# Kernel optimization log

Hardware: AMD Instinct MI355X
Metric: run time of the kernel (lower is better)

Reference implementation:

```python
import jax, jax.numpy as jnp
from jax import lax
import numpy as np

S, B, HP, WP, CIN, CO, DS, DI, K = 6, 1, 37, 37, 1536, 256, 16, 512, 4
N = HP * WP          # 1369 patches (37x37 grid)
OH, OW = 148, 148
HID = max(S * CO // 4, S)  # 384, attention hidden


def setup_inputs() -> dict:
    key = jax.random.key(0)
    ks = iter(jax.random.split(key, 64))
    def nrm(shape, scale):
        return jax.random.normal(next(ks), shape, jnp.float32) * scale
    inp = {}
    inp["features"] = nrm((S, B, 1, N, CIN), 1.0)
    # AdaptiveFusionModule (global branch)
    inp["proj_w"] = nrm((S, CO, CIN), CIN ** -0.5)          # per-source 1x1 conv
    inp["attn_w1"] = nrm((S * CO, HID), (S * CO) ** -0.5)
    inp["attn_b1"] = jnp.zeros((HID,), jnp.float32)
    inp["attn_w2"] = nrm((HID, S), HID ** -0.5)
    inp["attn_b2"] = jnp.zeros((S,), jnp.float32)
    inp["src_scale"] = jnp.ones((S,), jnp.float32)
    # two SelectiveSSM parameter sets (fwd / bwd scan)
    def ssm_params(tag):
        d = {}
        d[tag + "_in_w"] = nrm((CO, 2 * DI), CO ** -0.5)
        d[tag + "_conv_w"] = nrm((K, DI), K ** -0.5)         # depthwise causal conv
        d[tag + "_conv_b"] = jnp.zeros((DI,), jnp.float32)
        d[tag + "_xp_w"] = nrm((DI, 2 * DS + DI + 1), 0.02)  # B, C, delta, dt_bias
        # trained A_log; scaled so the log-domain cumsum stays in fp32 range over L=1369
        d[tag + "_Alog"] = jnp.log(jnp.arange(1, DS + 1, dtype=jnp.float32) / 1000.0) * jnp.ones((DI, 1), jnp.float32)
        d[tag + "_D"] = jnp.ones((DI,), jnp.float32)
        d[tag + "_out_w"] = nrm((DI, CO), DI ** -0.5)
        d[tag + "_ln_g"] = jnp.ones((CO,), jnp.float32)
        d[tag + "_ln_b"] = jnp.zeros((CO,), jnp.float32)
        return d
    inp.update(ssm_params("f"))
    inp.update(ssm_params("b"))
    inp["merge_w"] = nrm((2 * CO, CO), (2 * CO) ** -0.5)     # MSSR merge 1x1 conv
    inp["co1_w"] = nrm((3, 3, CO, CO), (9 * CO) ** -0.5)     # conv_out1, HWIO
    inp["co1_b"] = jnp.zeros((CO,), jnp.float32)
    inp["hp"], inp["wp"], inp["out_h"], inp["out_w"] = HP, WP, OH, OW
    return inp


def _causal_dwconv(z, w, b):
    # z: [B,L,D], w: [K,D] -> torch Conv1d(groups=D, padding=K-1)[..., :L]
    Kk, L = w.shape[0], z.shape[1]
    zp = jnp.pad(z, ((0, 0), (Kk - 1, 0), (0, 0)))
    return sum(zp[:, k:k + L, :] * w[k] for k in range(Kk)) + b


def _ssm(x, in_w, conv_w, conv_b, xp_w, Alog, D, out_w, ln_g, ln_b):
    # x: [B,L,d_model] -> [B,L,d_model]
    z, gate = jnp.split(x @ in_w, 2, axis=-1)               # [B,L,DI] each
    z = jax.nn.silu(_causal_dwconv(z, conv_w, conv_b))
    xp = z @ xp_w                                           # [B,L,2*DS+DI+1]
    ds = Alog.shape[1]
    Bp, Cp = xp[..., :ds], xp[..., ds:2 * ds]
    delta = jax.nn.softplus(xp[..., 2 * ds:-1] + xp[..., -1:])  # [B,L,DI]
    dA = jnp.exp(delta[..., None] * (-jnp.exp(Alog)))       # [B,L,DI,DS]
    dBu = delta[..., None] * Bp[:, :, None, :] * z[..., None]
    # log-domain cumsum scan: h[t] = sum_s exp(cs[t]-cs[s]) * dBu[s]
    cs = jnp.cumsum(jnp.log(jnp.clip(dA, 1e-38)), axis=1)
    h = jnp.exp(cs) * jnp.cumsum(jnp.exp(-cs) * dBu, axis=1)
    y = (h * Cp[:, :, None, :]).sum(-1) + D * z             # [B,L,DI]
    y = (y * jax.nn.silu(gate)) @ out_w                     # [B,L,d_model]
    r = y + x                                               # residual + LayerNorm
    mu = r.mean(-1, keepdims=True)
    v = ((r - mu) ** 2).mean(-1, keepdims=True)
    return ln_g * (r - mu) * lax.rsqrt(v + 1e-5) + ln_b


def _forward(features, proj_w, attn_w1, attn_b1, attn_w2, attn_b2, src_scale,
             f_in_w, f_conv_w, f_conv_b, f_xp_w, f_Alog, f_D, f_out_w, f_ln_g, f_ln_b,
             b_in_w, b_conv_w, b_conv_b, b_xp_w, b_Alog, b_D, b_out_w, b_ln_g, b_ln_b,
             merge_w, co1_w, co1_b, hp, wp, out_h, out_w):
    feats = features[:, :, 0]                               # [S,B,N,Cin]
    pf = jnp.einsum('sbnc,soc->sbno', feats, proj_w)        # [S,B,N,Co] per-source 1x1 proj
    Bsz = pf.shape[1]
    concat = pf.mean(2).transpose(1, 0, 2).reshape(Bsz, -1)  # [B,S*Co] pooled concat
    w = jax.nn.softmax(jax.nn.relu(concat @ attn_w1 + attn_b1) @ attn_w2 + attn_b2, axis=-1)
    w = jax.nn.softmax(w * src_scale, axis=-1)              # double softmax as in torch
    fused = jnp.einsum('bs,sbnc->bnc', w, pf)               # [B,N,Co]
    # MSSR bidirectional scan over row-major flattened patches
    fwd = _ssm(fused, f_in_w, f_conv_w, f_conv_b, f_xp_w, f_Alog, f_D, f_out_w, f_ln_g, f_ln_b)
    bwd = _ssm(fused[:, ::-1], b_in_w, b_conv_w, b_conv_b, b_xp_w, b_Alog, b_D, b_out_w, b_ln_g, b_ln_b)[:, ::-1]
    out = jnp.concatenate([fwd, bwd], axis=-1) @ merge_w    # [B,N,Co]
    sp = out.reshape(Bsz, hp, wp, -1)                       # NHWC
    up = jax.image.resize(sp, (Bsz, out_h, out_w, sp.shape[-1]), method='bilinear')
    y = lax.conv_general_dilated(up, co1_w, (1, 1), 'SAME',
                                 dimension_numbers=('NHWC', 'HWIO', 'NHWC')) + co1_b
    return y.transpose(0, 3, 1, 2)                          # [B,Co,out_h,out_w]


def reference(features, proj_w, attn_w1, attn_b1, attn_w2, attn_b2, src_scale,
              f_in_w, f_conv_w, f_conv_b, f_xp_w, f_Alog, f_D, f_out_w, f_ln_g, f_ln_b,
              b_in_w, b_conv_w, b_conv_b, b_xp_w, b_Alog, b_D, b_out_w, b_ln_g, b_ln_b,
              merge_w, co1_w, co1_b, hp, wp, out_h, out_w):
    return _forward(features, proj_w, attn_w1, attn_b1, attn_w2, attn_b2, src_scale,
                    f_in_w, f_conv_w, f_conv_b, f_xp_w, f_Alog, f_D, f_out_w, f_ln_g, f_ln_b,
                    b_in_w, b_conv_w, b_conv_b, b_xp_w, b_Alog, b_D, b_out_w, b_ln_g, b_ln_b,
                    merge_w, co1_w, co1_b, hp, wp, out_h, out_w)
```

## Files before the change

kernel.cpp:

```cpp
#include <hip/hip_runtime.h>
#include <math.h>


namespace {
constexpr int kS   = 6;
constexpr int kHP  = 37;
constexpr int kWP  = 37;
constexpr int kN   = 1369;
constexpr int kCIN = 1536;
constexpr int kCO  = 256;
constexpr int kDS  = 16;
constexpr int kDI  = 512;
constexpr int kHID = 384;
constexpr int kOH  = 148;
constexpr int kOW  = 148;
constexpr int kNP  = kOH * kOW;
constexpr int kXPW = 545;
constexpr long kXPS = 746112;
constexpr int kNC  = 48;
constexpr int kCH  = 29;

constexpr long OFF_PF      = 0;
constexpr long OFF_Z2B     = 0;
constexpr long OFF_YGB     = 0;
constexpr long OFF_UPB     = 0;
constexpr long OFF_SCANP   = 700928;
constexpr long OFF_SCANH   = 1487360;
constexpr long OFF_COLPART = 2102784;
constexpr long OFF_WFIN    = 2119680;
constexpr long OFF_ATTNP   = 2119696;
constexpr long OFF_PROJWB  = 2200000;
constexpr long OFF_INWT    = 2200000;
constexpr long OFF_FUSEDB  = 2462144;
constexpr long OFF_ZG      = 2820624;
constexpr long OFF_Z       = 5760000;
constexpr long OFF_WCONVB  = 6000000;
constexpr long OFF_FEATB   = 7161856;
constexpr long OFF_XP      = 7161856;
constexpr long OFF_DELTA   = 8654080;
constexpr long OFF_OUTWT   = 10055936;
constexpr long OFF_GT      = 11457792;
constexpr long OFF_XPWT    = 11457792;
constexpr long OFF_FUSED2  = 12158720;
constexpr long OFF_CAT     = 12859648;
constexpr long OFF_MERGEWT = 13210112;
constexpr long OFF_MERGED  = 13560576;
}

typedef __attribute__((ext_vector_type(8))) short bf16x8;
typedef __attribute__((ext_vector_type(4))) float f32x4;

__device__ __forceinline__ short f2bf(float x) {
    unsigned u = __builtin_bit_cast(unsigned, x);
    unsigned r = u + 0x7fffu + ((u >> 16) & 1u);
    return (short)(r >> 16);
}

__device__ __forceinline__ bf16x8 cvt8(float4 x, float4 y) {
    union { short s[8]; bf16x8 v; } u;
    u.s[0] = f2bf(x.x); u.s[1] = f2bf(x.y); u.s[2] = f2bf(x.z); u.s[3] = f2bf(x.w);
    u.s[4] = f2bf(y.x); u.s[5] = f2bf(y.y); u.s[6] = f2bf(y.z); u.s[7] = f2bf(y.w);
    return u.v;
}

__global__ __launch_bounds__(256)
void cast8_kernel(const float* __restrict__ in, short* __restrict__ out, long n8)
{
    long i = (long)blockIdx.x * 256 + threadIdx.x;
    if (i >= n8) return;
    const float4* p = (const float4*)(in + i * 8);
    *(bf16x8*)(out + i * 8) = cvt8(p[0], p[1]);
}

__global__ __launch_bounds__(256)
void transpose_cast_kernel(const float* __restrict__ w0, const float* __restrict__ w1,
                           short* __restrict__ wt, int K, int N)
{
    __shared__ float tile[32][33];
    int dir = blockIdx.z;
    const float* w = dir ? w1 : w0;
    short* o = wt + (long)dir * K * N;
    int k0 = blockIdx.x * 32, n0 = blockIdx.y * 32;
    int tx = threadIdx.x & 31, ty = threadIdx.x >> 5;
    #pragma unroll
    for (int r = 0; r < 32; r += 8) {
        int k = k0 + ty + r, n = n0 + tx;
        tile[ty + r][tx] = (k < K && n < N) ? w[(long)k * N + n] : 0.f;
    }
    __syncthreads();
    #pragma unroll
    for (int r = 0; r < 32; r += 8) {
        int n = n0 + ty + r, k = k0 + tx;
        if (n < N && k < K) o[(long)n * K + k] = f2bf(tile[tx][ty + r]);
    }
}

__global__ __launch_bounds__(256)
void mfma_nt(const short* __restrict__ A, long sA,
             const short* __restrict__ B, long sB,
             float* __restrict__ C, long sC,
             int M, int N, int K)
{
    __shared__ short smem[2][8192];
    const int bz = blockIdx.z;
    const short* Ab = A + (long)bz * sA;
    const short* Bb = B + (long)bz * sB;
    float* Cb = C + (long)bz * sC;
    const int t = threadIdx.x, w = t >> 6, l = t & 63;
    const int lr = l & 15, sg = l >> 4;
    const int m0 = blockIdx.x * 64, n0 = blockIdx.y * 64;

    const int srow = t >> 3, qa = t & 7;
    long gA[2]; int woffA[2];
    #pragma unroll
    for (int j = 0; j < 2; ++j) {
        int ar = srow + j * 32;
        int am = m0 + ar; if (am >= M) am = M - 1;
        gA[j] = (long)am * K + qa * 8;
        woffA[j] = ar * 128 + ((qa ^ (ar & 7)) << 4);
    }
    long gB[2]; int woffB[2];
    #pragma unroll
    for (int j = 0; j < 2; ++j) {
        int br = srow + j * 32;
        int bn = n0 + br; if (bn >= N) bn = N - 1;
        gB[j] = (long)bn * K + qa * 8;
        woffB[j] = 8192 + br * 128 + ((qa ^ (br & 7)) << 4);
    }

    int aoff[2][2], boff[2][2];
    #pragma unroll
    for (int mi = 0; mi < 2; ++mi) {
        int r = (w >> 1) * 32 + mi * 16 + lr;
        #pragma unroll
        for (int kk = 0; kk < 2; ++kk)
            aoff[mi][kk] = r * 128 + (((kk * 4 + sg) ^ (r & 7)) << 4);
    }
    #pragma unroll
    for (int ni = 0; ni < 2; ++ni) {
        int r = (w & 1) * 32 + ni * 16 + lr;
        #pragma unroll
        for (int kk = 0; kk < 2; ++kk)
            boff[ni][kk] = 8192 + r * 128 + (((kk * 4 + sg) ^ (r & 7)) << 4);
    }

    f32x4 acc[2][2] = {};
    const int NT = K >> 6;
    {
        char* lb = (char*)&smem[0][0];
        #pragma unroll
        for (int j = 0; j < 2; ++j)
            *(bf16x8*)(lb + woffA[j]) = *(const bf16x8*)(Ab + gA[j]);
        #pragma unroll
        for (int j = 0; j < 2; ++j)
            *(bf16x8*)(lb + woffB[j]) = *(const bf16x8*)(Bb + gB[j]);
    }
    __syncthreads();
    for (int tt = 0; tt < NT; ++tt) {
        bf16x8 nsa[2], nsb[2];
        if (tt + 1 < NT) {
            long o = (long)(tt + 1) * 64;
            #pragma unroll
            for (int j = 0; j < 2; ++j) nsa[j] = *(const bf16x8*)(Ab + gA[j] + o);
            #pragma unroll
            for (int j = 0; j < 2; ++j) nsb[j] = *(const bf16x8*)(Bb + gB[j] + o);
        }
        char* lb = (char*)&smem[tt & 1][0];
        #pragma unroll
        for (int kk = 0; kk < 2; ++kk) {
            bf16x8 a[2], b[2];
            #pragma unroll
            for (int mi = 0; mi < 2; ++mi) a[mi] = *(const bf16x8*)(lb + aoff[mi][kk]);
            #pragma unroll
            for (int ni = 0; ni < 2; ++ni) b[ni] = *(const bf16x8*)(lb + boff[ni][kk]);
            #pragma unroll
            for (int mi = 0; mi < 2; ++mi)
                #pragma unroll
                for (int ni = 0; ni < 2; ++ni)
                    acc[mi][ni] = __builtin_amdgcn_mfma_f32_16x16x32_bf16(a[mi], b[ni], acc[mi][ni], 0, 0, 0);
        }
        if (tt + 1 < NT) {
            char* nb = (char*)&smem[(tt + 1) & 1][0];
            #pragma unroll
            for (int j = 0; j < 2; ++j) *(bf16x8*)(nb + woffA[j]) = nsa[j];
            #pragma unroll
            for (int j = 0; j < 2; ++j) *(bf16x8*)(nb + woffB[j]) = nsb[j];
        }
        __syncthreads();
    }
    const int q = l >> 4;
    const int wm0 = m0 + (w >> 1) * 32, wn0 = n0 + (w & 1) * 32;
    #pragma unroll
    for (int mi = 0; mi < 2; ++mi)
        #pragma unroll
        for (int ni = 0; ni < 2; ++ni)
            #pragma unroll
            for (int r = 0; r < 4; ++r) {
                int m = wm0 + mi * 16 + q * 4 + r;
                int n = wn0 + ni * 16 + lr;
                if (m < M && n < N)
                    Cb[(long)m * N + n] = acc[mi][ni][r];
            }
}

__global__ __launch_bounds__(256)
void proj_mfma_kernel(const short* __restrict__ Ab16, const short* __restrict__ Bb16,
                      float* __restrict__ pf)
{
    __shared__ short smem[2][8192];
    const int bid = blockIdx.x;
    const int slot = (bid & 7) * 66 + (bid >> 3);
    const int s = slot / 88, rem = slot - s * 88;
    const int m0 = (rem >> 2) * 64, n0 = (rem & 3) * 64;
    const short* A = Ab16 + (long)s * kN * kCIN;
    const short* B = Bb16 + (long)s * kCO * kCIN;
    float* C = pf + (long)s * kN * kCO;
    const int t = threadIdx.x, w = t >> 6, l = t & 63;
    const int lr = l & 15, sg = l >> 4;

    const int srow = t >> 3, qa = t & 7;
    long gA[2]; int woffA[2];
    #pragma unroll
    for (int j = 0; j < 2; ++j) {
        int ar = srow + j * 32;
        int am = m0 + ar; if (am >= kN) am = kN - 1;
        gA[j] = (long)am * kCIN + qa * 8;
        woffA[j] = ar * 128 + ((qa ^ (ar & 7)) << 4);
    }
    long gB[2]; int woffB[2];
    #pragma unroll
    for (int j = 0; j < 2; ++j) {
        int br = srow + j * 32;
        gB[j] = (long)(n0 + br) * kCIN + qa * 8;
        woffB[j] = 8192 + br * 128 + ((qa ^ (br & 7)) << 4);
    }

    int aoff[2][2], boff[2][2];
    #pragma unroll
    for (int mi = 0; mi < 2; ++mi) {
        int r = (w >> 1) * 32 + mi * 16 + lr;
        #pragma unroll
        for (int kk = 0; kk < 2; ++kk)
            aoff[mi][kk] = r * 128 + (((kk * 4 + sg) ^ (r & 7)) << 4);
    }
    #pragma unroll
    for (int ni = 0; ni < 2; ++ni) {
        int r = (w & 1) * 32 + ni * 16 + lr;
        #pragma unroll
        for (int kk = 0; kk < 2; ++kk)
            boff[ni][kk] = 8192 + r * 128 + (((kk * 4 + sg) ^ (r & 7)) << 4);
    }

    f32x4 acc[2][2] = {};
    const int NT = kCIN >> 6;
    {
        char* lb = (char*)&smem[0][0];
        #pragma unroll
        for (int j = 0; j < 2; ++j)
            *(bf16x8*)(lb + woffA[j]) = *(const bf16x8*)(A + gA[j]);
        #pragma unroll
        for (int j = 0; j < 2; ++j)
            *(bf16x8*)(lb + woffB[j]) = *(const bf16x8*)(B + gB[j]);
    }
    __syncthreads();
    for (int tt = 0; tt < NT; ++tt) {
        bf16x8 nsa[2], nsb[2];
        if (tt + 1 < NT) {
            long o = (long)(tt + 1) * 64;
            #pragma unroll
            for (int j = 0; j < 2; ++j) nsa[j] = *(const bf16x8*)(A + gA[j] + o);
            #pragma unroll
            for (int j = 0; j < 2; ++j) nsb[j] = *(const bf16x8*)(B + gB[j] + o);
        }
        char* lb = (char*)&smem[tt & 1][0];
        #pragma unroll
        for (int kk = 0; kk < 2; ++kk) {
            bf16x8 a[2], b[2];
            #pragma unroll
            for (int mi = 0; mi < 2; ++mi) a[mi] = *(const bf16x8*)(lb + aoff[mi][kk]);
            #pragma unroll
            for (int ni = 0; ni < 2; ++ni) b[ni] = *(const bf16x8*)(lb + boff[ni][kk]);
            #pragma unroll
            for (int mi = 0; mi < 2; ++mi)
                #pragma unroll
                for (int ni = 0; ni < 2; ++ni)
                    acc[mi][ni] = __builtin_amdgcn_mfma_f32_16x16x32_bf16(a[mi], b[ni], acc[mi][ni], 0, 0, 0);
        }
        if (tt + 1 < NT) {
            char* nb = (char*)&smem[(tt + 1) & 1][0];
            #pragma unroll
            for (int j = 0; j < 2; ++j) *(bf16x8*)(nb + woffA[j]) = nsa[j];
            #pragma unroll
            for (int j = 0; j < 2; ++j) *(bf16x8*)(nb + woffB[j]) = nsb[j];
        }
        __syncthreads();
    }
    const int q = l >> 4;
    const int wm0 = m0 + (w >> 1) * 32, wn0 = n0 + (w & 1) * 32;
    #pragma unroll
    for (int mi = 0; mi < 2; ++mi)
        #pragma unroll
        for (int ni = 0; ni < 2; ++ni)
            #pragma unroll
            for (int r = 0; r < 4; ++r) {
                int m = wm0 + mi * 16 + q * 4 + r;
                if (m < kN)
                    C[(long)m * kCO + wn0 + ni * 16 + lr] = acc[mi][ni][r];
            }
}

__global__ __launch_bounds__(256)
void conv_mfma_kernel(const short* __restrict__ up, const short* __restrict__ wt,
                      const float* __restrict__ bias, float* __restrict__ out)
{
    __shared__ short smem[2][12288];
    const int t = threadIdx.x, w = t >> 6, l = t & 63;
    const int lr = l & 15, sg = l >> 4;
    const int bid = blockIdx.x;
    const int xcd = bid & 7, slot = bid >> 3;
    const int wgid = (xcd < 6 ? xcd * 86 : 6 * 86 + (xcd - 6) * 85) + slot;
    const int pm0 = (wgid >> 1) * 64;
    const int bn0 = (wgid & 1) * 128;

    const int srow = t >> 3, qa = t & 7;
    long gA[2]; int woffA[2];
    #pragma unroll
    for (int j = 0; j < 2; ++j) {
        int ar = srow + j * 32;
        int p = pm0 + ar; if (p >= kNP) p = kNP - 1;
        int oy = p / kOW, ox = p - oy * kOW;
        gA[j] = ((long)oy * 150 + ox) * kCO + qa * 8;
        woffA[j] = ar * 128 + ((qa ^ (ar & 7)) << 4);
    }
    long gB[4]; int woffB[4];
    #pragma unroll
    for (int j = 0; j < 4; ++j) {
        int br = srow + j * 32;
        gB[j] = (long)(bn0 + br) * 2304 + qa * 8;
        woffB[j] = 8192 + br * 128 + ((qa ^ (br & 7)) << 4);
    }

    int aoff[2][2], boff[4][2];
    #pragma unroll
    for (int mi = 0; mi < 2; ++mi) {
        int r = (w >> 1) * 32 + mi * 16 + lr;
        #pragma unroll
        for (int kk = 0; kk < 2; ++kk)
            aoff[mi][kk] = r * 128 + (((kk * 4 + sg) ^ (r & 7)) << 4);
    }
    #pragma unroll
    for (int ni = 0; ni < 4; ++ni) {
        int r = (w & 1) * 64 + ni * 16 + lr;
        #pragma unroll
        for (int kk = 0; kk < 2; ++kk)
            boff[ni][kk] = 8192 + r * 128 + (((kk * 4 + sg) ^ (r & 7)) << 4);
    }

    f32x4 acc[2][4] = {};
    const int NT = 36;

#define CONV_BAR() { \
        asm volatile("s_waitcnt lgkmcnt(0)" ::: "memory"); \
        __builtin_amdgcn_sched_barrier(0); \
        __builtin_amdgcn_s_barrier(); }

#define CONV_TADDR(tn, ta, tb) { \
        int _tap = (tn) >> 2, _c0 = ((tn) & 3) << 6; \
        int _ky = _tap / 3, _kx = _tap - _ky * 3; \
        ta = ((long)_ky * 150 + _kx) * kCO + _c0; \
        tb = (long)(tn) * 64; }

#define CONV_LOAD(Pa_, Pb_, tn) { \
        long _ta, _tb; CONV_TADDR(tn, _ta, _tb); \
        _Pragma("unroll") \
        for (int j = 0; j < 2; ++j) Pa_[j] = *(const bf16x8*)(up + gA[j] + _ta); \
        _Pragma("unroll") \
        for (int j = 0; j < 4; ++j) Pb_[j] = *(const bf16x8*)(wt + gB[j] + _tb); }

#define CONV_WRITE(buf, Pa_, Pb_) { \
        char* _nb = (char*)&smem[buf][0]; \
        _Pragma("unroll") \
        for (int j = 0; j < 2; ++j) *(bf16x8*)(_nb + woffA[j]) = Pa_[j]; \
        _Pragma("unroll") \
        for (int j = 0; j < 4; ++j) *(bf16x8*)(_nb + woffB[j]) = Pb_[j]; }

#define CONV_COMPUTE(buf) { \
        char* _lb = (char*)&smem[buf][0]; \
        _Pragma("unroll") \
        for (int kk = 0; kk < 2; ++kk) { \
            bf16x8 _a[2], _b[4]; \
            _Pragma("unroll") \
            for (int mi = 0; mi < 2; ++mi) _a[mi] = *(const bf16x8*)(_lb + aoff[mi][kk]); \
            _Pragma("unroll") \
            for (int ni = 0; ni < 4; ++ni) _b[ni] = *(const bf16x8*)(_lb + boff[ni][kk]); \
            __builtin_amdgcn_s_setprio(1); \
            _Pragma("unroll") \
            for (int mi = 0; mi < 2; ++mi) \
                _Pragma("unroll") \
                for (int ni = 0; ni < 4; ++ni) \
                    acc[mi][ni] = __builtin_amdgcn_mfma_f32_16x16x32_bf16(_a[mi], _b[ni], acc[mi][ni], 0, 0, 0); \
            __builtin_amdgcn_s_setprio(0); \
        } }

    bf16x8 PaA[2], PaB[4];
    bf16x8 PbA[2], PbB[4];

    CONV_LOAD(PaA, PaB, 0);
    CONV_WRITE(0, PaA, PaB);
    CONV_LOAD(PbA, PbB, 1);
    CONV_BAR();

    for (int tt = 0; tt < NT; tt += 2) {
        if (tt + 2 < NT) CONV_LOAD(PaA, PaB, tt + 2);
        CONV_COMPUTE(0);
        CONV_WRITE(1, PbA, PbB);
        CONV_BAR();
        if (tt + 3 < NT) CONV_LOAD(PbA, PbB, tt + 3);
        CONV_COMPUTE(1);
        if (tt + 2 < NT) CONV_WRITE(0, PaA, PaB);
        CONV_BAR();
    }
#undef CONV_BAR
#undef CONV_TADDR
#undef CONV_LOAD
#undef CONV_WRITE
#undef CONV_COMPUTE

    const int q = l >> 4;
    const int m0 = pm0 + (w >> 1) * 32;
    const int n0 = bn0 + (w & 1) * 64;
    #pragma unroll
    for (int mi = 0; mi < 2; ++mi)
        #pragma unroll
        for (int ni = 0; ni < 4; ++ni) {
            const int co = n0 + ni * 16 + lr;
            const float bv = bias[co];
            #pragma unroll
            for (int r = 0; r < 4; ++r) {
                int p = m0 + mi * 16 + q * 4 + r;
                if (p < kNP)
                    out[(long)co * kNP + p] = acc[mi][ni][r] + bv;
            }
        }
}

__global__ __launch_bounds__(256)
void colmean_kernel(const float* __restrict__ pf, float* __restrict__ colpart)
{
    int s = blockIdx.x, ch = blockIdx.y, o = threadIdx.x;
    int n0 = ch * 128, n1 = n0 + 128 > kN ? kN : n0 + 128;
    float a = 0.f;
    for (int n = n0; n < n1; ++n) a += pf[((long)s * kN + n) * kCO + o];
    colpart[ch * kS * kCO + s * kCO + o] = a;
}

__global__ __launch_bounds__(384)
void attn_part1(const float* __restrict__ colpart, const float* __restrict__ w1,
                float* __restrict__ partial)
{
    __shared__ float cm[128];
    int b = blockIdx.x, t = threadIdx.x;
    int c0 = b * 128;
    if (t < 128) {
        float a = 0.f;
        #pragma unroll
        for (int ch = 0; ch < 11; ++ch) a += colpart[ch * kS * kCO + c0 + t];
        cm[t] = a * (1.f / kN);
    }
    __syncthreads();
    float acc = 0.f;
    #pragma unroll 4
    for (int c = 0; c < 128; ++c) acc += cm[c] * w1[(long)(c0 + c) * kHID + t];
    partial[b * kHID + t] = acc;
}

__global__ __launch_bounds__(384)
void attn_part2(const float* __restrict__ partial, const float* __restrict__ b1,
                const float* __restrict__ w2, const float* __restrict__ b2,
                const float* __restrict__ ss, float* __restrict__ wfin)
{
    __shared__ float h[kHID];
    __shared__ float logits[8];
    int t = threadIdx.x;
    float acc = b1[t];
    #pragma unroll
    for (int b = 0; b < 12; ++b) acc += partial[b * kHID + t];
    h[t] = fmaxf(acc, 0.f);
    __syncthreads();
    if (t < kS) {
        float lg = b2[t];
        for (int j = 0; j < kHID; ++j) lg += h[j] * w2[j * kS + t];
        logits[t] = lg;
    }
    __syncthreads();
    if (t == 0) {
        float w[kS], mx = -1e30f, sum = 0.f;
        for (int s = 0; s < kS; ++s) mx = fmaxf(mx, logits[s]);
        for (int s = 0; s < kS; ++s) { w[s] = expf(logits[s] - mx); sum += w[s]; }
        for (int s = 0; s < kS; ++s) w[s] /= sum;
        mx = -1e30f;
        for (int s = 0; s < kS; ++s) { w[s] *= ss[s]; mx = fmaxf(mx, w[s]); }
        sum = 0.f;
        float e[kS];
        for (int s = 0; s < kS; ++s) { e[s] = expf(w[s] - mx); sum += e[s]; }
        for (int s = 0; s < kS; ++s) wfin[s] = e[s] / sum;
    }
}

__global__ __launch_bounds__(256)
void fuse_kernel(const float* __restrict__ pf, const float* __restrict__ wfin,
                 float* __restrict__ fused, short* __restrict__ fusedb2)
{
    long idx = (long)blockIdx.x * 256 + threadIdx.x;
    if (idx >= (long)kN * kCO) return;
    float acc = 0.f;
    #pragma unroll
    for (int s = 0; s < kS; ++s) acc += wfin[s] * pf[(long)s * kN * kCO + idx];
    long n = idx / kCO; int c = (int)(idx % kCO);
    long ridx = (long)kN * kCO + (kN - 1 - n) * kCO + c;
    short bv = f2bf(acc);
    fused[idx] = acc;
    fusedb2[idx] = bv;
    fusedb2[ridx] = bv;
}

__global__ __launch_bounds__(256)
void dwconv_kernel(const float* __restrict__ zg2,
                   const float* __restrict__ wf, const float* __restrict__ bf,
                   const float* __restrict__ wb, const float* __restrict__ bb,
                   float* __restrict__ z2, short* __restrict__ z2b)
{
    long idx = (long)blockIdx.x * 256 + threadIdx.x;
    int dir = blockIdx.y;
    if (idx >= (long)kN * kDI) return;
    long n = idx >> 9; int i = (int)(idx & (kDI - 1));
    const float* zg = zg2 + (long)dir * kN * 2 * kDI;
    const float* w  = dir ? wb : wf;
    const float* b  = dir ? bb : bf;
    float acc = b[i];
    #pragma unroll
    for (int k = 0; k < 4; ++k) {
        long m = n - 3 + k;
        if (m >= 0) acc += w[k * kDI + i] * zg[m * 2 * kDI + i];
    }
    float sg = 1.f / (1.f + expf(-acc));
    float v = acc * sg;
    z2 [(long)dir * kN * kDI + idx] = v;
    z2b[(long)dir * kN * kDI + idx] = f2bf(v);
}

__global__ __launch_bounds__(256)
void delta_kernel(const float* __restrict__ xp2, float* __restrict__ delta2)
{
    long idx = (long)blockIdx.x * 256 + threadIdx.x;
    int dir = blockIdx.y;
    if (idx >= (long)kN * kDI) return;
    long n = idx >> 9; int i = (int)(idx & (kDI - 1));
    const float* xp = xp2 + (long)dir * kXPS + n * kXPW;
    float x = xp[2 * kDS + i] + xp[kXPW - 1];
    float sp = fmaxf(x, 0.f) + log1pf(expf(-fabsf(x)));
    delta2[(long)dir * kN * kDI + idx] = sp;
}

__global__ __launch_bounds__(256)
void scan_partA(const float* __restrict__ delta2, const float* __restrict__ z2,
                const float* __restrict__ xp2,
                const float* __restrict__ Alogf, const float* __restrict__ Alogb,
                float* __restrict__ chunkP, float* __restrict__ chunkH)
{
    int bx = blockIdx.x;
    int c  = blockIdx.y;
    int dir = bx >> 5, iblk = bx & 31;
    int t = threadIdx.x;
    int s = t & 15, il = t >> 4;
    int i = iblk * 16 + il;
    int gid = dir * 8192 + iblk * 256 + t;
    const float* Alog = dir ? Alogb : Alogf;
    float A = expf(Alog[i * kDS + s]);
    int n0 = c * kCH, n1 = n0 + kCH; if (n1 > kN) n1 = kN;
    const int cnt = n1 - n0;
    const float* dp = delta2 + (long)dir * kN * kDI + (long)n0 * kDI + i;
    const float* zp = z2     + (long)dir * kN * kDI + (long)n0 * kDI + i;
    const float* xpp = xp2   + (long)dir * kXPS     + (long)n0 * kXPW;

    float d0 = *dp, v0 = *zp, b0 = xpp[s];
    dp += kDI; zp += kDI; xpp += kXPW;
    float d1 = 0.f, v1 = 0.f, b1 = 0.f;
    if (cnt > 1) { d1 = *dp; v1 = *zp; b1 = xpp[s]; }

    float h = 0.f, P = 1.f;
    for (int k = 0; k < cnt; ++k) {
        dp += kDI; zp += kDI; xpp += kXPW;
        float d2 = 0.f, v2 = 0.f, b2 = 0.f;
        if (k + 2 < cnt) { d2 = *dp; v2 = *zp; b2 = xpp[s]; }
        float dA = __expf(-d0 * A);
        h = dA * h + d0 * b0 * v0;
        P *= dA;
        d0 = d1; v0 = v1; b0 = b1;
        d1 = d2; v1 = v2; b1 = b2;
    }
    chunkP[(long)c * 16384 + gid] = P;
    chunkH[(long)c * 16384 + gid] = h;
}

__global__ __launch_bounds__(256)
void scan_partB(float* __restrict__ chunkP, const float* __restrict__ chunkH)
{
    int gid = blockIdx.x * 256 + threadIdx.x;
    float P0 = chunkP[gid];
    float Q0 = chunkH[gid];
    float P1 = chunkP[16384L + gid];
    float Q1 = chunkH[16384L + gid];
    float H = 0.f;
    for (int c = 0; c < kNC; ++c) {
        float P2 = 0.f, Q2 = 0.f;
        if (c + 2 < kNC) {
            P2 = chunkP[(long)(c + 2) * 16384 + gid];
            Q2 = chunkH[(long)(c + 2) * 16384 + gid];
        }
        chunkP[(long)c * 16384 + gid] = H;
        H = P0 * H + Q0;
        P0 = P1; Q0 = Q1;
        P1 = P2; Q1 = Q2;
    }
}

__global__ __launch_bounds__(256)
void scan_partC(const float* __restrict__ delta2, const float* __restrict__ z2,
                const float* __restrict__ xp2, const float* __restrict__ zg2,
                const float* __restrict__ Df, const float* __restrict__ Db,
                const float* __restrict__ Alogf, const float* __restrict__ Alogb,
                const float* __restrict__ hin, short* __restrict__ ygb)
{
    int bx = blockIdx.x;
    int c  = blockIdx.y;
    int dir = bx >> 5, iblk = bx & 31;
    int t = threadIdx.x;
    int s = t & 15, il = t >> 4;
    int i = iblk * 16 + il;
    int gid = dir * 8192 + iblk * 256 + t;
    const float* D    = dir ? Db : Df;
    const float* Alog = dir ? Alogb : Alogf;
    float A  = expf(Alog[i * kDS + s]);
    float Dv = D[i];
    int n0 = c * kCH, n1 = n0 + kCH; if (n1 > kN) n1 = kN;
    const int cnt = n1 - n0;
    const float* dp  = delta2 + (long)dir * kN * kDI + (long)n0 * kDI + i;
    const float* zp  = z2     + (long)dir * kN * kDI + (long)n0 * kDI + i;
    const float* xpp = xp2    + (long)dir * kXPS     + (long)n0 * kXPW;
    const float* gp  = zg2    + (long)dir * kN * 2 * kDI + (long)n0 * 2 * kDI + kDI + i;
    short* yp        = ygb    + (long)dir * kN * kDI + (long)n0 * kDI + i;

    float d0 = *dp, v0 = *zp, b0 = xpp[s], c0 = xpp[kDS + s];
    float g0 = 0.f; if (s == 0) g0 = *gp;
    dp += kDI; zp += kDI; xpp += kXPW; gp += 2 * kDI;
    float d1 = 0.f, v1 = 0.f, b1 = 0.f, c1 = 0.f, g1 = 0.f;
    if (cnt > 1) {
        d1 = *dp; v1 = *zp; b1 = xpp[s]; c1 = xpp[kDS + s];
        if (s == 0) g1 = *gp;
    }

    float h = hin[(long)c * 16384 + gid];
    for (int k = 0; k < cnt; ++k) {
        dp += kDI; zp += kDI; xpp += kXPW; gp += 2 * kDI;
        float d2 = 0.f, v2 = 0.f, b2 = 0.f, c2 = 0.f, g2 = 0.f;
        if (k + 2 < cnt) {
            d2 = *dp; v2 = *zp; b2 = xpp[s]; c2 = xpp[kDS + s];
            if (s == 0) g2 = *gp;
        }
        float dA = __expf(-d0 * A);
        h = dA * h + d0 * b0 * v0;
        float cc = h * c0;
        cc += __shfl_xor(cc, 1, 16);
        cc += __shfl_xor(cc, 2, 16);
        cc += __shfl_xor(cc, 4, 16);
        cc += __shfl_xor(cc, 8, 16);
        if (s == 0) {
            float sgm = 1.f / (1.f + __expf(-g0));
            float v = (cc + Dv * v0) * g0 * sgm;
            *yp = f2bf(v);
        }
        yp += kDI;
        d0 = d1; v0 = v1; b0 = b1; c0 = c1; g0 = g1;
        d1 = d2; v1 = v2; b1 = b2; c1 = c2; g1 = g2;
    }
}

__global__ __launch_bounds__(256)
void resid_ln_cat_kernel(const float* __restrict__ gt2, const float* __restrict__ fused,
                         const float* __restrict__ gf, const float* __restrict__ betf,
                         const float* __restrict__ gb, const float* __restrict__ betb,
                         short* __restrict__ catb)
{
    int n = blockIdx.x, dir = blockIdx.y, t = threadIdx.x;
    const float* gt = gt2 + ((long)dir * kN + n) * kCO;
    int xrow = dir ? (kN - 1 - n) : n;
    const float* x  = fused + (long)xrow * kCO;
    const float* g  = dir ? gb : gf;
    const float* be = dir ? betb : betf;
    float r = gt[t] + x[t];
    float s1 = r, s2 = r * r;
    #pragma unroll
    for (int m = 32; m >= 1; m >>= 1) {
        s1 += __shfl_xor(s1, m, 64);
        s2 += __shfl_xor(s2, m, 64);
    }
    __shared__ float red[8];
    int w = t >> 6;
    if ((t & 63) == 0) { red[w] = s1; red[4 + w] = s2; }
    __syncthreads();
    float S1 = red[0] + red[1] + red[2] + red[3];
    float S2 = red[4] + red[5] + red[6] + red[7];
    float mu  = S1 * (1.f / kCO);
    float var = S2 * (1.f / kCO) - mu * mu;
    float inv = rsqrtf(var + 1e-5f);
    float v = g[t] * (r - mu) * inv + be[t];
    int row = dir ? (kN - 1 - n) : n;
    catb[(long)row * (2 * kCO) + dir * kCO + t] = f2bf(v);
}

__global__ __launch_bounds__(256)
void upsample_kernel(const float* __restrict__ merged, short* __restrict__ up)
{
    int p = blockIdx.x;
    int y = p / 150, x = p - y * 150;
    int c = threadIdx.x;
    if (y == 0 || y == 149 || x == 0 || x == 149) {
        up[((long)y * 150 + x) * kCO + c] = 0;
        return;
    }
    int oy = y - 1, ox = x - 1;
    float sy = (oy + 0.5f) * ((float)kHP / (float)kOH) - 0.5f;
    float sx = (ox + 0.5f) * ((float)kWP / (float)kOW) - 0.5f;
    int iy0 = (int)floorf(sy); float fy = sy - (float)iy0;
    int ix0 = (int)floorf(sx); float fx = sx - (float)ix0;
    float wy0 = 1.f - fy, wy1 = fy, wx0 = 1.f - fx, wx1 = fx;
    int iy1 = iy0 + 1, ix1 = ix0 + 1;
    if (iy0 < 0)       { iy0 = 0;       wy0 = 0.f; }
    if (iy1 > kHP - 1) { iy1 = kHP - 1; wy1 = 0.f; }
    if (ix0 < 0)       { ix0 = 0;       wx0 = 0.f; }
    if (ix1 > kWP - 1) { ix1 = kWP - 1; wx1 = 0.f; }
    float wys = wy0 + wy1; wy0 /= wys; wy1 /= wys;
    float wxs = wx0 + wx1; wx0 /= wxs; wx1 /= wxs;
    const float* M00 = merged + (long)(iy0 * kWP + ix0) * kCO;
    const float* M01 = merged + (long)(iy0 * kWP + ix1) * kCO;
    const float* M10 = merged + (long)(iy1 * kWP + ix0) * kCO;
    const float* M11 = merged + (long)(iy1 * kWP + ix1) * kCO;
    float v = wy0 * (wx0 * M00[c] + wx1 * M01[c]) + wy1 * (wx0 * M10[c] + wx1 * M11[c]);
    up[((long)y * 150 + x) * kCO + c] = f2bf(v);
}

extern "C" void kernel_launch(void* const* d_in, const int* in_sizes, int n_in,
                              void* d_out, int out_size, void* d_ws, size_t ws_size,
                              hipStream_t stream)
{
    (void)in_sizes; (void)n_in; (void)out_size; (void)ws_size;
    const float* features  = (const float*)d_in[0];
    const float* proj_w    = (const float*)d_in[1];
    const float* attn_w1   = (const float*)d_in[2];
    const float* attn_b1   = (const float*)d_in[3];
    const float* attn_w2   = (const float*)d_in[4];
    const float* attn_b2   = (const float*)d_in[5];
    const float* src_scale = (const float*)d_in[6];
    const float* f_in_w    = (const float*)d_in[7];
    const float* f_conv_w  = (const float*)d_in[8];
    const float* f_conv_b  = (const float*)d_in[9];
    const float* f_xp_w    = (const float*)d_in[10];
    const float* f_Alog    = (const float*)d_in[11];
    const float* f_D       = (const float*)d_in[12];
    const float* f_out_w   = (const float*)d_in[13];
    const float* f_ln_g    = (const float*)d_in[14];
    const float* f_ln_b    = (const float*)d_in[15];
    const float* b_in_w    = (const float*)d_in[16];
    const float* b_conv_w  = (const float*)d_in[17];
    const float* b_conv_b  = (const float*)d_in[18];
    const float* b_xp_w    = (const float*)d_in[19];
    const float* b_Alog    = (const float*)d_in[20];
    const float* b_D       = (const float*)d_in[21];
    const float* b_out_w   = (const float*)d_in[22];
    const float* b_ln_g    = (const float*)d_in[23];
    const float* b_ln_b    = (const float*)d_in[24];
    const float* merge_w   = (const float*)d_in[25];
    const float* co1_w     = (const float*)d_in[26];
    const float* co1_b     = (const float*)d_in[27];

    float* ws      = (float*)d_ws;
    float* outp    = (float*)d_out;
    float* pf      = ws + OFF_PF;
    float* colpart = ws + OFF_COLPART;
    float* wfin    = ws + OFF_WFIN;
    float* attnp   = ws + OFF_ATTNP;
    float* fused   = ws + OFF_FUSED2;
    float* zg2     = ws + OFF_ZG;
    float* z2      = ws + OFF_Z;
    float* xp2     = ws + OFF_XP;
    float* delta2  = ws + OFF_DELTA;
    float* gt2     = ws + OFF_GT;
    float* merged  = ws + OFF_MERGED;
    float* chunkP  = ws + OFF_SCANP;
    float* chunkH  = ws + OFF_SCANH;
    short* featb   = (short*)(ws + OFF_FEATB);
    short* projwb  = (short*)(ws + OFF_PROJWB);
    short* in_wt   = (short*)(ws + OFF_INWT);
    short* xp_wt   = (short*)(ws + OFF_XPWT);
    short* out_wt  = (short*)(ws + OFF_OUTWT);
    short* mrg_wt  = (short*)(ws + OFF_MERGEWT);
    short* fusedb2 = (short*)(ws + OFF_FUSEDB);
    short* z2b     = (short*)(ws + OFF_Z2B);
    short* ygb     = (short*)(ws + OFF_YGB);
    short* catb    = (short*)(ws + OFF_CAT);
    short* upb     = (short*)(ws + OFF_UPB);
    short* wconvb  = (short*)(ws + OFF_WCONVB);

    cast8_kernel<<<dim3(6161), 256, 0, stream>>>(features, featb, 1577088L);
    cast8_kernel<<<dim3(1152), 256, 0, stream>>>(proj_w, projwb, 294912L);
    proj_mfma_kernel<<<dim3(528), 256, 0, stream>>>(featb, projwb, pf);
    transpose_cast_kernel<<<dim3(8, 32, 2), 256, 0, stream>>>(f_in_w, b_in_w, in_wt, 256, 1024);
    transpose_cast_kernel<<<dim3(16, 18, 2), 256, 0, stream>>>(f_xp_w, b_xp_w, xp_wt, 512, 545);
    transpose_cast_kernel<<<dim3(16, 8, 1), 256, 0, stream>>>(merge_w, merge_w, mrg_wt, 512, 256);
    colmean_kernel<<<dim3(6, 11), 256, 0, stream>>>(pf, colpart);
    attn_part1<<<dim3(12), 384, 0, stream>>>(colpart, attn_w1, attnp);
    attn_part2<<<1, 384, 0, stream>>>(attnp, attn_b1, attn_w2, attn_b2, src_scale, wfin);
    fuse_kernel<<<dim3(1369), 256, 0, stream>>>(pf, wfin, fused, fusedb2);
    transpose_cast_kernel<<<dim3(16, 8, 2), 256, 0, stream>>>(f_out_w, b_out_w, out_wt, 512, 256);
    mfma_nt<<<dim3(22, 16, 2), 256, 0, stream>>>(
        fusedb2, (long)kN * kCO, in_wt, (long)2 * kDI * kCO,
        zg2, (long)kN * 2 * kDI, kN, 2 * kDI, kCO);
    dwconv_kernel<<<dim3(2738, 2), 256, 0, stream>>>(zg2, f_conv_w, f_conv_b,
                                                     b_conv_w, b_conv_b, z2, z2b);
    mfma_nt<<<dim3(22, 9, 2), 256, 0, stream>>>(
        z2b, (long)kN * kDI, xp_wt, (long)kXPW * kDI,
        xp2, kXPS, kN, kXPW, kDI);
    delta_kernel<<<dim3(2738, 2), 256, 0, stream>>>(xp2, delta2);
    scan_partA<<<dim3(64, kNC), 256, 0, stream>>>(delta2, z2, xp2, f_Alog, b_Alog,
                                                  chunkP, chunkH);
    scan_partB<<<dim3(64), 256, 0, stream>>>(chunkP, chunkH);
    scan_partC<<<dim3(64, kNC), 256, 0, stream>>>(delta2, z2, xp2, zg2, f_D, b_D,
                                                  f_Alog, b_Alog, chunkP, ygb);
    mfma_nt<<<dim3(22, 4, 2), 256, 0, stream>>>(
        ygb, (long)kN * kDI, out_wt, (long)kCO * kDI,
        gt2, (long)kN * kCO, kN, kCO, kDI);
    resid_ln_cat_kernel<<<dim3(1369, 2), 256, 0, stream>>>(gt2, fused, f_ln_g, f_ln_b,
                                                           b_ln_g, b_ln_b, catb);
    mfma_nt<<<dim3(22, 4, 1), 256, 0, stream>>>(
        catb, 0, mrg_wt, 0,
        merged, 0, kN, kCO, 2 * kCO);
    transpose_cast_kernel<<<dim3(72, 8, 1), 256, 0, stream>>>(co1_w, co1_w, wconvb, 2304, 256);
    upsample_kernel<<<dim3(150 * 150), 256, 0, stream>>>(merged, upb);
    conv_mfma_kernel<<<dim3(686), 256, 0, stream>>>(upb, wconvb, co1_b, outp);
}
```

Baseline: 282.2 us.

## Fuse fp32-to-bf16 casts into projection GEMM and batch weight transposes

Removes the two standalone cast kernels for the features and projection weights. The projection GEMM now loads fp32 directly and converts to bf16 while staging into shared memory, which avoids writing and re-reading a bf16 copy of the 8.4M-element feature tensor. The five separate weight transpose-cast launches are merged into one launch of 2048 blocks, so fewer kernels run on the stream. In exchange the GEMM reads twice the bytes per tile from global memory, and the conv weight buffer moves to a new workspace offset.

```diff
diff --git a/kernel.cpp b/kernel.cpp
--- a/kernel.cpp
+++ b/kernel.cpp
@@ -29,16 +29,14 @@
 constexpr long OFF_COLPART = 2102784;
 constexpr long OFF_WFIN    = 2119680;
 constexpr long OFF_ATTNP   = 2119696;
-constexpr long OFF_PROJWB  = 2200000;
 constexpr long OFF_INWT    = 2200000;
 constexpr long OFF_FUSEDB  = 2462144;
 constexpr long OFF_ZG      = 2820624;
 constexpr long OFF_Z       = 5760000;
-constexpr long OFF_WCONVB  = 6000000;
-constexpr long OFF_FEATB   = 7161856;
 constexpr long OFF_XP      = 7161856;
 constexpr long OFF_DELTA   = 8654080;
 constexpr long OFF_OUTWT   = 10055936;
+constexpr long OFF_WCONVB  = 10500000;
 constexpr long OFF_GT      = 11457792;
 constexpr long OFF_XPWT    = 11457792;
 constexpr long OFF_FUSED2  = 12158720;
@@ -64,24 +62,42 @@
 }
 
 __global__ __launch_bounds__(256)
-void cast8_kernel(const float* __restrict__ in, short* __restrict__ out, long n8)
-{
-    long i = (long)blockIdx.x * 256 + threadIdx.x;
-    if (i >= n8) return;
-    const float4* p = (const float4*)(in + i * 8);
-    *(bf16x8*)(out + i * 8) = cvt8(p[0], p[1]);
-}
-
-__global__ __launch_bounds__(256)
-void transpose_cast_kernel(const float* __restrict__ w0, const float* __restrict__ w1,
-                           short* __restrict__ wt, int K, int N)
-{
+void batched_transpose_kernel(
+    const float* __restrict__ f_in_w, const float* __restrict__ b_in_w, short* __restrict__ in_wt,
+    const float* __restrict__ f_xp_w, const float* __restrict__ b_xp_w, short* __restrict__ xp_wt,
+    const float* __restrict__ merge_w, short* __restrict__ mrg_wt,
+    const float* __restrict__ f_out_w, const float* __restrict__ b_out_w, short* __restrict__ out_wt,
+    const float* __restrict__ co1_w, short* __restrict__ wconvb)
+{
+    const int bid = blockIdx.x;
+    const float* w; short* o; int K, N, tk, tn;
+    if (bid < 512) {
+        int dir = bid >> 8, r = bid & 255;
+        K = 256; N = 1024;
+        w = dir ? b_in_w : f_in_w; o = in_wt + (long)dir * K * N;
+        tk = r >> 5; tn = r & 31;
+    } else if (bid < 1088) {
+        int r = bid - 512; int dir = r / 288; r -= dir * 288;
+        K = 512; N = 545;
+        w = dir ? b_xp_w : f_xp_w; o = xp_wt + (long)dir * K * N;
+        tk = r / 18; tn = r - tk * 18;
+    } else if (bid < 1216) {
+        int r = bid - 1088;
+        K = 512; N = 256; w = merge_w; o = mrg_wt;
+        tk = r >> 3; tn = r & 7;
+    } else if (bid < 1472) {
+        int r = bid - 1216; int dir = r >> 7; r &= 127;
+        K = 512; N = 256;
+        w = dir ? b_out_w : f_out_w; o = out_wt + (long)dir * K * N;
+        tk = r >> 3; tn = r & 7;
+    } else {
+        int r = bid - 1472;
+        K = 2304; N = 256; w = co1_w; o = wconvb;
+        tk = r >> 3; tn = r & 7;
+    }
+    const int k0 = tk * 32, n0 = tn * 32;
     __shared__ float tile[32][33];
-    int dir = blockIdx.z;
-    const float* w = dir ? w1 : w0;
-    short* o = wt + (long)dir * K * N;
-    int k0 = blockIdx.x * 32, n0 = blockIdx.y * 32;
-    int tx = threadIdx.x & 31, ty = threadIdx.x >> 5;
+    const int tx = threadIdx.x & 31, ty = threadIdx.x >> 5;
     #pragma unroll
     for (int r = 0; r < 32; r += 8) {
         int k = k0 + ty + r, n = n0 + tx;
@@ -204,7 +220,7 @@
 }
 
 __global__ __launch_bounds__(256)
-void proj_mfma_kernel(const short* __restrict__ Ab16, const short* __restrict__ Bb16,
+void proj_mfma_kernel(const float* __restrict__ Af, const float* __restrict__ Bf,
                       float* __restrict__ pf)
 {
     __shared__ short smem[2][8192];
@@ -212,8 +228,8 @@
     const int slot = (bid & 7) * 66 + (bid >> 3);
     const int s = slot / 88, rem = slot - s * 88;
     const int m0 = (rem >> 2) * 64, n0 = (rem & 3) * 64;
-    const short* A = Ab16 + (long)s * kN * kCIN;
-    const short* B = Bb16 + (long)s * kCO * kCIN;
+    const float* A = Af + (long)s * kN * kCIN;
+    const float* B = Bf + (long)s * kCO * kCIN;
     float* C = pf + (long)s * kN * kCO;
     const int t = threadIdx.x, w = t >> 6, l = t & 63;
     const int lr = l & 15, sg = l >> 4;
@@ -256,21 +272,33 @@
     {
         char* lb = (char*)&smem[0][0];
         #pragma unroll
-        for (int j = 0; j < 2; ++j)
-            *(bf16x8*)(lb + woffA[j]) = *(const bf16x8*)(A + gA[j]);
-        #pragma unroll
-        for (int j = 0; j < 2; ++j)
-            *(bf16x8*)(lb + woffB[j]) = *(const bf16x8*)(B + gB[j]);
+        for (int j = 0; j < 2; ++j) {
+            float4 x = *(const float4*)(A + gA[j]);
+            float4 y = *(const float4*)(A + gA[j] + 4);
+            *(bf16x8*)(lb + woffA[j]) = cvt8(x, y);
+        }
+        #pragma unroll
+        for (int j = 0; j < 2; ++j) {
+            float4 x = *(const float4*)(B + gB[j]);
+            float4 y = *(const float4*)(B + gB[j] + 4);
+            *(bf16x8*)(lb + woffB[j]) = cvt8(x, y);
+        }
     }
     __syncthreads();
     for (int tt = 0; tt < NT; ++tt) {
-        bf16x8 nsa[2], nsb[2];
+        float4 na0[2], na1[2], nb0[2], nb1[2];
         if (tt + 1 < NT) {
             long o = (long)(tt + 1) * 64;
             #pragma unroll
-            for (int j = 0; j < 2; ++j) nsa[j] = *(const bf16x8*)(A + gA[j] + o);
-            #pragma unroll
-            for (int j = 0; j < 2; ++j) nsb[j] = *(const bf16x8*)(B + gB[j] + o);
+            for (int j = 0; j < 2; ++j) {
+                na0[j] = *(const float4*)(A + gA[j] + o);
+                na1[j] = *(const float4*)(A + gA[j] + o + 4);
+            }
+            #pragma unroll
+            for (int j = 0; j < 2; ++j) {
+                nb0[j] = *(const float4*)(B + gB[j] + o);
+                nb1[j] = *(const float4*)(B + gB[j] + o + 4);
+            }
         }
         char* lb = (char*)&smem[tt & 1][0];
         #pragma unroll
@@ -289,9 +317,9 @@
         if (tt + 1 < NT) {
             char* nb = (char*)&smem[(tt + 1) & 1][0];
             #pragma unroll
-            for (int j = 0; j < 2; ++j) *(bf16x8*)(nb + woffA[j]) = nsa[j];
-            #pragma unroll
-            for (int j = 0; j < 2; ++j) *(bf16x8*)(nb + woffB[j]) = nsb[j];
+            for (int j = 0; j < 2; ++j) *(bf16x8*)(nb + woffA[j]) = cvt8(na0[j], na1[j]);
+            #pragma unroll
+            for (int j = 0; j < 2; ++j) *(bf16x8*)(nb + woffB[j]) = cvt8(nb0[j], nb1[j]);
         }
         __syncthreads();
     }
@@ -799,8 +827,6 @@
     float* merged  = ws + OFF_MERGED;
     float* chunkP  = ws + OFF_SCANP;
     float* chunkH  = ws + OFF_SCANH;
-    short* featb   = (short*)(ws + OFF_FEATB);
-    short* projwb  = (short*)(ws + OFF_PROJWB);
     short* in_wt   = (short*)(ws + OFF_INWT);
     short* xp_wt   = (short*)(ws + OFF_XPWT);
     short* out_wt  = (short*)(ws + OFF_OUTWT);
@@ -812,17 +838,14 @@
     short* upb     = (short*)(ws + OFF_UPB);
     short* wconvb  = (short*)(ws + OFF_WCONVB);
 
-    cast8_kernel<<<dim3(6161), 256, 0, stream>>>(features, featb, 1577088L);
-    cast8_kernel<<<dim3(1152), 256, 0, stream>>>(proj_w, projwb, 294912L);
-    proj_mfma_kernel<<<dim3(528), 256, 0, stream>>>(featb, projwb, pf);
-    transpose_cast_kernel<<<dim3(8, 32, 2), 256, 0, stream>>>(f_in_w, b_in_w, in_wt, 256, 1024);
-    transpose_cast_kernel<<<dim3(16, 18, 2), 256, 0, stream>>>(f_xp_w, b_xp_w, xp_wt, 512, 545);
-    transpose_cast_kernel<<<dim3(16, 8, 1), 256, 0, stream>>>(merge_w, merge_w, mrg_wt, 512, 256);
+    batched_transpose_kernel<<<dim3(2048), 256, 0, stream>>>(
+        f_in_w, b_in_w, in_wt, f_xp_w, b_xp_w, xp_wt,
+        merge_w, mrg_wt, f_out_w, b_out_w, out_wt, co1_w, wconvb);
+    proj_mfma_kernel<<<dim3(528), 256, 0, stream>>>(features, proj_w, pf);
     colmean_kernel<<<dim3(6, 11), 256, 0, stream>>>(pf, colpart);
     attn_part1<<<dim3(12), 384, 0, stream>>>(colpart, attn_w1, attnp);
     attn_part2<<<1, 384, 0, stream>>>(attnp, attn_b1, attn_w2, attn_b2, src_scale, wfin);
     fuse_kernel<<<dim3(1369), 256, 0, stream>>>(pf, wfin, fused, fusedb2);
-    transpose_cast_kernel<<<dim3(16, 8, 2), 256, 0, stream>>>(f_out_w, b_out_w, out_wt, 512, 256);
     mfma_nt<<<dim3(22, 16, 2), 256, 0, stream>>>(
         fusedb2, (long)kN * kCO, in_wt, (long)2 * kDI * kCO,
         zg2, (long)kN * 2 * kDI, kN, 2 * kDI, kCO);
@@ -845,7 +868,6 @@
     mfma_nt<<<dim3(22, 4, 1), 256, 0, stream>>>(
         catb, 0, mrg_wt, 0,
         merged, 0, kN, kCO, 2 * kCO);
-    transpose_cast_kernel<<<dim3(72, 8, 1), 256, 0, stream>>>(co1_w, co1_w, wconvb, 2304, 256);
     upsample_kernel<<<dim3(150 * 150), 256, 0, stream>>>(merged, upb);
     conv_mfma_kernel<<<dim3(686), 256, 0, stream>>>(upb, wconvb, co1_b, outp);
 }
```

Result: no change. 280.0 us (-0.8%).
